# Performance work log

Hardware: AMD Instinct MI355X
Metric: run time of the kernel (lower is better)

The kernel has to match this reference:

```python
import jax, jax.numpy as jnp
import numpy as np

DIM = 1024
NUM_HEADS = 16
HEAD_DIM = DIM // NUM_HEADS
EPS = 1e-6


def _rmsnorm(x, w):
    # x: [B,H,N,D], w: [D]
    var = jnp.mean(x * x, axis=-1, keepdims=True)
    return x * jax.lax.rsqrt(var + EPS) * w


def _rotary(x, cos, sin):
    # x: [B,H,N,D]; cos/sin: [1,1,N,D/2]; complex-pair rotation (llama style)
    x2 = x.reshape(*x.shape[:-1], HEAD_DIM // 2, 2)
    xr, xi = x2[..., 0], x2[..., 1]
    or_ = xr * cos - xi * sin
    oi_ = xr * sin + xi * cos
    return jnp.stack([or_, oi_], axis=-1).reshape(x.shape)


def setup_inputs() -> dict:
    key = jax.random.key(0)
    ks = jax.random.split(key, 6)
    B, N = 2, 2048
    x = jax.random.normal(ks[0], (B, N, DIM), dtype=jnp.float32)
    pos = jax.random.uniform(ks[1], (N, HEAD_DIM // 2), dtype=jnp.float32)  # rotary angles
    s_in = 1.0 / np.sqrt(DIM)
    qkv_w = jax.random.normal(ks[2], (3 * DIM, DIM), dtype=jnp.float32) * s_in
    q_norm_w = jnp.ones((HEAD_DIM,), dtype=jnp.float32)
    k_norm_w = jnp.ones((HEAD_DIM,), dtype=jnp.float32)
    proj_w = jax.random.normal(ks[3], (DIM, DIM), dtype=jnp.float32) * s_in
    proj_b = jnp.zeros((DIM,), dtype=jnp.float32)
    return {"x": x, "pos": pos, "qkv_w": qkv_w, "q_norm_w": q_norm_w,
            "k_norm_w": k_norm_w, "proj_w": proj_w, "proj_b": proj_b}


def reference(x, pos, qkv_w, q_norm_w, k_norm_w, proj_w, proj_b):
    B, N, C = x.shape
    H, D = NUM_HEADS, HEAD_DIM
    scale = D ** -0.5
    # QKV projection: [B,N,3C] -> [3,B,H,N,D]
    qkv = jnp.einsum('bnc,fc->bnf', x, qkv_w)
    qkv = qkv.reshape(B, N, 3, H, D).transpose(2, 0, 3, 1, 4)
    q, k, v = qkv[0], qkv[1], qkv[2]
    # QK RMSNorm over head_dim
    q = _rmsnorm(q, q_norm_w)
    k = _rmsnorm(k, k_norm_w)
    # Rotary embedding (freqs_cis = exp(i * pos))
    cos = jnp.cos(pos)[None, None, :, :]
    sin = jnp.sin(pos)[None, None, :, :]
    q = _rotary(q, cos, sin)
    k = _rotary(k, cos, sin)
    # Scaled dot-product attention (non-causal)
    scores = jnp.einsum('bhnd,bhmd->bhnm', q, k) * scale
    attn = jax.nn.softmax(scores, axis=-1)
    out = jnp.einsum('bhnm,bhmd->bhnd', attn, v)
    out = out.transpose(0, 2, 1, 3).reshape(B, N, C)
    return jnp.einsum('bnc,oc->bno', out, proj_w) + proj_b
```

## Files before the change

### kernel.cpp

```cpp
#include <hip/hip_runtime.h>
#include <hip/hip_bf16.h>

typedef unsigned short ushort_t;
using floatx4 = __attribute__((__ext_vector_type__(4))) float;
using bf16x8  = __attribute__((__ext_vector_type__(8))) __bf16;
using ushort4v = __attribute__((__ext_vector_type__(4))) ushort_t;

__device__ __forceinline__ unsigned int pkbf(float a, float b) {
  __hip_bfloat162 h = __float22bfloat162_rn(make_float2(a, b));
  unsigned int u;
  __builtin_memcpy(&u, &h, 4);
  return u;
}

__device__ __forceinline__ void gl2lds16(const ushort_t* g, ushort_t* l) {
  __builtin_amdgcn_global_load_lds(
      (const __attribute__((address_space(1))) unsigned int*)g,
      (__attribute__((address_space(3))) unsigned int*)l, 16, 0, 0);
}

__global__ void cast_all(const float* __restrict__ x, const float* __restrict__ qw,
                         const float* __restrict__ pw, ushort_t* __restrict__ ob,
                         const float* __restrict__ pos, float* __restrict__ cs) {
  const int T1 = 4096 * 1024, T2 = T1 + 3072 * 1024, T3 = T2 + 1024 * 1024;
  const int tid = blockIdx.x * blockDim.x + threadIdx.x;
  if (tid < 65536) {
    const float a = pos[tid];
    cs[2 * tid]     = __cosf(a);
    cs[2 * tid + 1] = __sinf(a);
  }
  const int i = tid * 4;
  if (i < T3) {
    const float* src = (i < T1) ? (x + i) : (i < T2) ? (qw + (i - T1)) : (pw + (i - T2));
    float4 v = *reinterpret_cast<const float4*>(src);
    uint2 o = make_uint2(pkbf(v.x, v.y), pkbf(v.z, v.w));
    *reinterpret_cast<uint2*>(&ob[i]) = o;
  }
}

__global__ __launch_bounds__(256)
void gemm_qkv_fused(const ushort_t* __restrict__ A, const ushort_t* __restrict__ B,
                    const float* __restrict__ cs,
                    const float* __restrict__ qnw, const float* __restrict__ knw,
                    ushort_t* __restrict__ qr, ushort_t* __restrict__ kr,
                    ushort_t* __restrict__ vt) {
  const int K = 1024;
  __shared__ ushort_t sA[128 * 32];
  __shared__ ushort_t sB[128 * 32];
  __shared__ __align__(16) ushort_t sE[4][4096];
  const int m0 = blockIdx.y * 128, n0 = blockIdx.x * 128;
  const int tid = threadIdx.x;
  const int lane = tid & 63, w = tid >> 6;
  const int wm = (w >> 1) * 64;
  const int grp = lane >> 4, l16 = lane & 15;
  const int r0 = lane >> 2, c0 = (lane & 3) * 8;
  floatx4 acc[4][4] = {};
  for (int k0 = 0; k0 < K; k0 += 32) {
    __syncthreads();
#pragma unroll
    for (int i = 0; i < 2; i++) {
      const int j = w * 2 + i;
      gl2lds16(&A[(size_t)(m0 + j * 16 + r0) * K + k0 + c0], &sA[j * 512]);
      gl2lds16(&B[(size_t)(n0 + j * 16 + r0) * K + k0 + c0], &sB[j * 512]);
    }
    __syncthreads();
    bf16x8 af[4], bfr[4];
#pragma unroll
    for (int i = 0; i < 4; i++)
      af[i] = *reinterpret_cast<const bf16x8*>(&sA[(wm + i * 16 + l16) * 32 + grp * 8]);
#pragma unroll
    for (int i = 0; i < 4; i++)
      bfr[i] = *reinterpret_cast<const bf16x8*>(&sB[((w & 1) * 64 + i * 16 + l16) * 32 + grp * 8]);
#pragma unroll
    for (int i = 0; i < 4; i++)
#pragma unroll
      for (int j = 0; j < 4; j++)
        acc[i][j] = __builtin_amdgcn_mfma_f32_16x16x32_bf16(af[i], bfr[j], acc[i][j], 0, 0, 0);
  }
  const int region = n0 >> 10;
  const int h = ((n0 & 1023) >> 6) + (w & 1);
  const int tbase = m0 + wm;
  const int bb = tbase >> 11;
  const int nwin = tbase & 2047;
  const int q = lane & 7;
  const int lr = lane >> 3;

  if (region < 2) {
    float* sEf = (float*)&sE[w][0];
    const float* nwp = (region == 0) ? qnw : knw;
    const float qmul = (region == 0) ? 0.125f * 1.44269504088896340736f : 1.0f;
    float wgt[8];
    *(float4*)&wgt[0] = *(const float4*)&nwp[q * 8];
    *(float4*)&wgt[4] = *(const float4*)&nwp[q * 8 + 4];
#pragma unroll
    for (int hf = 0; hf < 2; hf++) {
      __syncthreads();
#pragma unroll
      for (int i2 = 0; i2 < 2; i2++)
#pragma unroll
        for (int rr = 0; rr < 4; rr++) {
          const int t2 = i2 * 16 + grp * 4 + rr;
#pragma unroll
          for (int j = 0; j < 4; j++) {
            const int cd = (j * 4 + (l16 >> 2)) ^ (t2 & 15);
            sEf[t2 * 64 + cd * 4 + (l16 & 3)] = acc[hf * 2 + i2][j][rr];
          }
        }
      __syncthreads();
#pragma unroll
      for (int tg = 0; tg < 4; tg++) {
        const int t2 = tg * 8 + lr;
        const int n = (tbase + hf * 32 + t2) & 2047;
        float v0[8];
        const int ck1 = (2 * q) ^ (t2 & 15), ck2 = (2 * q + 1) ^ (t2 & 15);
        *(float4*)&v0[0] = *(const float4*)&sEf[t2 * 64 + ck1 * 4];
        *(float4*)&v0[4] = *(const float4*)&sEf[t2 * 64 + ck2 * 4];
        float ss = 0.f;
#pragma unroll
        for (int e = 0; e < 8; e++) ss += v0[e] * v0[e];
        ss += __shfl_xor(ss, 1); ss += __shfl_xor(ss, 2); ss += __shfl_xor(ss, 4);
        const float rn = rsqrtf(ss * (1.0f / 64.0f) + 1e-6f);
        float4 c01 = *(const float4*)&cs[(n * 32 + q * 4) * 2];
        float4 c23 = *(const float4*)&cs[(n * 32 + q * 4) * 2 + 4];
        float ccv[4] = {c01.x, c01.z, c23.x, c23.z};
        float snv[4] = {c01.y, c01.w, c23.y, c23.w};
        union { unsigned int u32[4]; uint4 v4; } ov;
#pragma unroll
        for (int p = 0; p < 4; p++) {
          const float cc = ccv[p], sn = snv[p];
          const float xr = v0[2 * p] * rn * wgt[2 * p];
          const float xi = v0[2 * p + 1] * rn * wgt[2 * p + 1];
          ov.u32[p] = pkbf((xr * cc - xi * sn) * qmul, (xr * sn + xi * cc) * qmul);
        }
        const size_t rowb = ((size_t)(bb * 16 + h) * 2048 + n) * 64;
        if (region == 0)
          *reinterpret_cast<uint4*>(&qr[rowb + q * 8]) = ov.v4;
        else
          *reinterpret_cast<uint4*>(&kr[rowb + (q ^ (n & 7)) * 8]) = ov.v4;
      }
    }
  } else {
    __syncthreads();
#pragma unroll
    for (int i = 0; i < 4; i++)
#pragma unroll
      for (int j = 0; j < 4; j++) {
        const int d = j * 16 + l16;
        const int ct = (i * 4 + grp) ^ (d & 15);
        uint2 pk = make_uint2(pkbf(acc[i][j][0], acc[i][j][1]),
                              pkbf(acc[i][j][2], acc[i][j][3]));
        *reinterpret_cast<uint2*>(&sE[w][d * 64 + ct * 4]) = pk;
      }
    __syncthreads();
#pragma unroll
    for (int dd = 0; dd < 8; dd++) {
      const int d = dd * 8 + lr;
      const int cta = 8 * (q >> 2) + (q & 3);
      union { ushort4v h[2]; uint4 v4; } ob;
      ob.h[0] = *reinterpret_cast<const ushort4v*>(&sE[w][d * 64 + ((cta ^ (d & 15)) * 4)]);
      ob.h[1] = *reinterpret_cast<const ushort4v*>(&sE[w][d * 64 + (((cta + 4) ^ (d & 15)) * 4)]);
      *reinterpret_cast<uint4*>(
          &vt[((size_t)(bb * 16 + h) * 64 + d) * 2048 + nwin + (q ^ (d & 7)) * 8]) = ob.v4;
    }
  }
}

__global__ __launch_bounds__(256)
void flash_attn(const ushort_t* __restrict__ qr, const ushort_t* __restrict__ kr,
                const ushort_t* __restrict__ vt, ushort_t* __restrict__ aout) {
  const int bh = blockIdx.y;
  const int w = threadIdx.x >> 6, lane = threadIdx.x & 63;
  const int grp = lane >> 4, l16 = lane & 15;
  const int sw = l16 & 7;
  const int q0 = blockIdx.x * 128 + w * 32;
  const size_t hb = (size_t)bh * 2048 * 64;

  __shared__ ushort_t sK[2][128 * 64];
  __shared__ ushort_t sV[2][64 * 128];

  bf16x8 qa[2][2];
#pragma unroll
  for (int f = 0; f < 2; f++) {
    const ushort_t* qp = &qr[hb + (size_t)(q0 + f * 16 + l16) * 64 + grp * 8];
    qa[f][0] = *reinterpret_cast<const bf16x8*>(qp);
    qa[f][1] = *reinterpret_cast<const bf16x8*>(qp + 32);
  }

  floatx4 o[2][4] = {};
  floatx4 ol[2] = {};

  union { ushort_t u[8]; bf16x8 v; } onef;
#pragma unroll
  for (int e = 0; e < 8; e++) onef.u[e] = 0x3F80;

  auto stage = [&](int buf, int k0) {
    const ushort_t* kg = &kr[hb + (size_t)k0 * 64];
#pragma unroll
    for (int i = 0; i < 4; i++) {
      const int j = w * 4 + i;
      gl2lds16(kg + j * 512 + lane * 8, &sK[buf][j * 512]);
    }
#pragma unroll
    for (int i = 0; i < 4; i++) {
      const int d = w * 16 + i * 4;
      gl2lds16(&vt[((size_t)bh * 64 + d + (lane >> 4)) * 2048 + k0 + (lane & 15) * 8],
               &sV[buf][d * 128]);
    }
  };

  stage(0, 0);
  const int g0 = (grp ^ sw) * 8;
  for (int it = 0; it < 16; it++) {
    const int cur = it & 1;
    __syncthreads();
    if (it + 1 < 16) stage(1 - cur, (it + 1) * 128);
#pragma unroll
    for (int hh = 0; hh < 2; hh++) {
      const ushort_t* kb = &sK[cur][hh * 64 * 64];
      const ushort_t* vb = &sV[cur][hh * 64];
      floatx4 s[2][4];
#pragma unroll
      for (int nt = 0; nt < 4; nt++) {
        const ushort_t* kp = kb + (nt * 16 + l16) * 64;
        bf16x8 kf0 = *reinterpret_cast<const bf16x8*>(kp + g0);
        bf16x8 kf1 = *reinterpret_cast<const bf16x8*>(kp + (g0 ^ 32));
#pragma unroll
        for (int f = 0; f < 2; f++) {
          floatx4 acc = {};
          acc = __builtin_amdgcn_mfma_f32_16x16x32_bf16(kf0, qa[f][0], acc, 0, 0, 0);
          acc = __builtin_amdgcn_mfma_f32_16x16x32_bf16(kf1, qa[f][1], acc, 0, 0, 0);
          s[f][nt] = acc;
        }
      }
      union { unsigned int u32[4]; bf16x8 v; } pf[2][2];
#pragma unroll
      for (int f = 0; f < 2; f++) {
        float p[4][4];
#pragma unroll
        for (int nt = 0; nt < 4; nt++)
#pragma unroll
          for (int r = 0; r < 4; r++)
            p[nt][r] = __builtin_amdgcn_exp2f(s[f][nt][r]);
#pragma unroll
        for (int c = 0; c < 2; c++) {
          pf[f][c].u32[0] = pkbf(p[2 * c][0], p[2 * c][1]);
          pf[f][c].u32[1] = pkbf(p[2 * c][2], p[2 * c][3]);
          pf[f][c].u32[2] = pkbf(p[2 * c + 1][0], p[2 * c + 1][1]);
          pf[f][c].u32[3] = pkbf(p[2 * c + 1][2], p[2 * c + 1][3]);
        }
      }
#pragma unroll
      for (int c = 0; c < 2; c++) {
#pragma unroll
        for (int f = 0; f < 2; f++)
          ol[f] = __builtin_amdgcn_mfma_f32_16x16x32_bf16(onef.v, pf[f][c].v, ol[f], 0, 0, 0);
#pragma unroll
        for (int dt = 0; dt < 4; dt++) {
          const bf16x8 vv = *reinterpret_cast<const bf16x8*>(
              vb + (dt * 16 + l16) * 128 + (((c * 4 + grp) ^ sw) << 3));
#pragma unroll
          for (int f = 0; f < 2; f++)
            o[f][dt] = __builtin_amdgcn_mfma_f32_16x16x32_bf16(vv, pf[f][c].v, o[f][dt], 0, 0, 0);
        }
      }
    }
  }
  const int b = bh >> 4, h = bh & 15;
#pragma unroll
  for (int f = 0; f < 2; f++) {
    const float rl = 1.0f / ol[f][0];
    const size_t orow = (size_t)(b * 2048 + q0 + f * 16 + l16) * 1024 + h * 64;
#pragma unroll
    for (int dt = 0; dt < 4; dt++) {
      uint2 ov = make_uint2(pkbf(o[f][dt][0] * rl, o[f][dt][1] * rl),
                            pkbf(o[f][dt][2] * rl, o[f][dt][3] * rl));
      *reinterpret_cast<uint2*>(&aout[orow + dt * 16 + grp * 4]) = ov;
    }
  }
}

__global__ __launch_bounds__(256)
void gemm_proj(const ushort_t* __restrict__ A, const ushort_t* __restrict__ B,
               float* __restrict__ Cout, const float* __restrict__ bias) {
  const int K = 1024, N = 1024;
  __shared__ ushort_t sA[128 * 32];
  __shared__ ushort_t sB[64 * 32];
  __shared__ float sT[4][2048];
  const int m0 = blockIdx.y * 128, n0 = blockIdx.x * 64;
  const int tid = threadIdx.x;
  const int lane = tid & 63, w = tid >> 6;
  const int wm = (w >> 1) * 64, wn = (w & 1) * 32;
  const int grp = lane >> 4, l16 = lane & 15;
  const int r0 = lane >> 2, c0 = (lane & 3) * 8;
  floatx4 acc[4][2] = {};
  for (int k0 = 0; k0 < K; k0 += 32) {
    __syncthreads();
#pragma unroll
    for (int i = 0; i < 2; i++) {
      const int j = w * 2 + i;
      gl2lds16(&A[(size_t)(m0 + j * 16 + r0) * K + k0 + c0], &sA[j * 512]);
    }
    gl2lds16(&B[(size_t)(n0 + w * 16 + r0) * K + k0 + c0], &sB[w * 512]);
    __syncthreads();
    bf16x8 af[4], bfr[2];
#pragma unroll
    for (int i = 0; i < 4; i++)
      af[i] = *reinterpret_cast<const bf16x8*>(&sA[(wm + i * 16 + l16) * 32 + grp * 8]);
#pragma unroll
    for (int j = 0; j < 2; j++)
      bfr[j] = *reinterpret_cast<const bf16x8*>(&sB[(wn + j * 16 + l16) * 32 + grp * 8]);
#pragma unroll
    for (int i = 0; i < 4; i++)
#pragma unroll
      for (int j = 0; j < 2; j++)
        acc[i][j] = __builtin_amdgcn_mfma_f32_16x16x32_bf16(af[i], bfr[j], acc[i][j], 0, 0, 0);
  }
  float bv[2];
#pragma unroll
  for (int j = 0; j < 2; j++) bv[j] = bias[n0 + wn + j * 16 + l16];
#pragma unroll
  for (int i = 0; i < 4; i++)
#pragma unroll
    for (int j = 0; j < 2; j++) {
      const int col = j * 16 + l16, c4 = col >> 2;
#pragma unroll
      for (int rr = 0; rr < 4; rr++) {
        const int row = i * 16 + grp * 4 + rr;
        sT[w][row * 32 + ((c4 ^ (row & 7)) << 2) + (col & 3)] = acc[i][j][rr] + bv[j];
      }
    }
  __builtin_amdgcn_s_waitcnt(0);
  const int lr = lane >> 3, ch = lane & 7;
#pragma unroll
  for (int rg = 0; rg < 8; rg++) {
    const int row = rg * 8 + lr;
    float4 vvv = *(const float4*)&sT[w][row * 32 + ((ch ^ (row & 7)) << 2)];
    *reinterpret_cast<float4*>(&Cout[(size_t)(m0 + wm + row) * N + n0 + wn + ch * 4]) = vvv;
  }
}

extern "C" void kernel_launch(void* const* d_in, const int* in_sizes, int n_in,
                              void* d_out, int out_size, void* d_ws, size_t ws_size,
                              hipStream_t stream) {
  const float* x      = (const float*)d_in[0];
  const float* pos    = (const float*)d_in[1];
  const float* qkv_w  = (const float*)d_in[2];
  const float* q_nw   = (const float*)d_in[3];
  const float* k_nw   = (const float*)d_in[4];
  const float* proj_w = (const float*)d_in[5];
  const float* proj_b = (const float*)d_in[6];
  float* out = (float*)d_out;

  ushort_t* x_b     = (ushort_t*)d_ws;
  ushort_t* qkvw_b  = x_b     + (size_t)4096 * 1024;
  ushort_t* projw_b = qkvw_b  + (size_t)3072 * 1024;
  ushort_t* q_r     = projw_b + (size_t)1024 * 1024;
  ushort_t* k_r     = q_r     + (size_t)32 * 2048 * 64;
  ushort_t* v_t     = k_r     + (size_t)32 * 2048 * 64;
  ushort_t* a_out   = v_t     + (size_t)32 * 2048 * 64;
  float*    cs_tab  = (float*)(a_out + (size_t)4096 * 1024);

  cast_all<<<8388608 / 4 / 256, 256, 0, stream>>>(x, qkv_w, proj_w, x_b, pos, cs_tab);

  gemm_qkv_fused<<<dim3(3072 / 128, 4096 / 128), 256, 0, stream>>>(
      x_b, qkvw_b, cs_tab, q_nw, k_nw, q_r, k_r, v_t);

  flash_attn<<<dim3(2048 / 128, 32), 256, 0, stream>>>(q_r, k_r, v_t, a_out);

  gemm_proj<<<dim3(1024 / 64, 4096 / 128), 256, 0, stream>>>(a_out, projw_b, out, proj_b);
}
```

Baseline: 214.3 us.

## Double GEMM K-step to 64 with XOR-swizzled LDS and alias epilogue scratch

Both the QKV and projection GEMMs now stage 64-wide K slices per iteration instead of 32, which halves the number of barrier pairs in the main loop. The LDS tiles use an XOR swizzle on the 16-byte chunks to avoid bank conflicts on the fragment reads. In the QKV kernel the epilogue scratch now aliases the A/B staging buffers, which cuts the kernel's shared memory footprint. Per-wave epilogue barriers become waitcnt, on the premise that each wave's region is private. The risk is that dropping the block barriers relies on wave-private LDS regions and on LDS ordering within a wave.

```diff
diff --git a/kernel.cpp b/kernel.cpp
--- a/kernel.cpp
+++ b/kernel.cpp
@@ -45,38 +45,50 @@
                     ushort_t* __restrict__ qr, ushort_t* __restrict__ kr,
                     ushort_t* __restrict__ vt) {
   const int K = 1024;
-  __shared__ ushort_t sA[128 * 32];
-  __shared__ ushort_t sB[128 * 32];
-  __shared__ __align__(16) ushort_t sE[4][4096];
+  __shared__ __align__(16) ushort_t smem[16384];
+  ushort_t* sA = smem;
+  ushort_t* sB = smem + 8192;
   const int m0 = blockIdx.y * 128, n0 = blockIdx.x * 128;
   const int tid = threadIdx.x;
   const int lane = tid & 63, w = tid >> 6;
   const int wm = (w >> 1) * 64;
   const int grp = lane >> 4, l16 = lane & 15;
-  const int r0 = lane >> 2, c0 = (lane & 3) * 8;
+  const int r8 = lane >> 3;
+  const int c8 = ((lane & 7) ^ r8) * 8;
   floatx4 acc[4][4] = {};
-  for (int k0 = 0; k0 < K; k0 += 32) {
-    __syncthreads();
-#pragma unroll
-    for (int i = 0; i < 2; i++) {
-      const int j = w * 2 + i;
-      gl2lds16(&A[(size_t)(m0 + j * 16 + r0) * K + k0 + c0], &sA[j * 512]);
-      gl2lds16(&B[(size_t)(n0 + j * 16 + r0) * K + k0 + c0], &sB[j * 512]);
-    }
-    __syncthreads();
-    bf16x8 af[4], bfr[4];
-#pragma unroll
-    for (int i = 0; i < 4; i++)
-      af[i] = *reinterpret_cast<const bf16x8*>(&sA[(wm + i * 16 + l16) * 32 + grp * 8]);
-#pragma unroll
-    for (int i = 0; i < 4; i++)
-      bfr[i] = *reinterpret_cast<const bf16x8*>(&sB[((w & 1) * 64 + i * 16 + l16) * 32 + grp * 8]);
-#pragma unroll
-    for (int i = 0; i < 4; i++)
-#pragma unroll
-      for (int j = 0; j < 4; j++)
-        acc[i][j] = __builtin_amdgcn_mfma_f32_16x16x32_bf16(af[i], bfr[j], acc[i][j], 0, 0, 0);
-  }
+  for (int k0 = 0; k0 < K; k0 += 64) {
+    __syncthreads();
+#pragma unroll
+    for (int i = 0; i < 4; i++) {
+      const int j = w * 4 + i;
+      gl2lds16(&A[(size_t)(m0 + j * 8 + r8) * K + k0 + c8], &sA[j * 512]);
+      gl2lds16(&B[(size_t)(n0 + j * 8 + r8) * K + k0 + c8], &sB[j * 512]);
+    }
+    __syncthreads();
+#pragma unroll
+    for (int kk = 0; kk < 2; kk++) {
+      bf16x8 af[4], bfr[4];
+#pragma unroll
+      for (int i = 0; i < 4; i++) {
+        const int ra = wm + i * 16 + l16;
+        af[i] = *reinterpret_cast<const bf16x8*>(
+            &sA[ra * 64 + (((kk * 4 + grp) ^ (ra & 7)) << 3)]);
+      }
+#pragma unroll
+      for (int i = 0; i < 4; i++) {
+        const int rb = (w & 1) * 64 + i * 16 + l16;
+        bfr[i] = *reinterpret_cast<const bf16x8*>(
+            &sB[rb * 64 + (((kk * 4 + grp) ^ (rb & 7)) << 3)]);
+      }
+#pragma unroll
+      for (int i = 0; i < 4; i++)
+#pragma unroll
+        for (int j = 0; j < 4; j++)
+          acc[i][j] = __builtin_amdgcn_mfma_f32_16x16x32_bf16(af[i], bfr[j], acc[i][j], 0, 0, 0);
+    }
+  }
+  __syncthreads();
+  ushort_t* sE = smem + w * 4096;
   const int region = n0 >> 10;
   const int h = ((n0 & 1023) >> 6) + (w & 1);
   const int tbase = m0 + wm;
@@ -86,7 +98,7 @@
   const int lr = lane >> 3;
 
   if (region < 2) {
-    float* sEf = (float*)&sE[w][0];
+    float* sEf = (float*)sE;
     const float* nwp = (region == 0) ? qnw : knw;
     const float qmul = (region == 0) ? 0.125f * 1.44269504088896340736f : 1.0f;
     float wgt[8];
@@ -94,7 +106,7 @@
     *(float4*)&wgt[4] = *(const float4*)&nwp[q * 8 + 4];
 #pragma unroll
     for (int hf = 0; hf < 2; hf++) {
-      __syncthreads();
+      __builtin_amdgcn_s_waitcnt(0);
 #pragma unroll
       for (int i2 = 0; i2 < 2; i2++)
 #pragma unroll
@@ -106,7 +118,7 @@
             sEf[t2 * 64 + cd * 4 + (l16 & 3)] = acc[hf * 2 + i2][j][rr];
           }
         }
-      __syncthreads();
+      __builtin_amdgcn_s_waitcnt(0);
 #pragma unroll
       for (int tg = 0; tg < 4; tg++) {
         const int t2 = tg * 8 + lr;
@@ -140,7 +152,6 @@
       }
     }
   } else {
-    __syncthreads();
 #pragma unroll
     for (int i = 0; i < 4; i++)
 #pragma unroll
@@ -149,16 +160,16 @@
         const int ct = (i * 4 + grp) ^ (d & 15);
         uint2 pk = make_uint2(pkbf(acc[i][j][0], acc[i][j][1]),
                               pkbf(acc[i][j][2], acc[i][j][3]));
-        *reinterpret_cast<uint2*>(&sE[w][d * 64 + ct * 4]) = pk;
-      }
-    __syncthreads();
+        *reinterpret_cast<uint2*>(&sE[d * 64 + ct * 4]) = pk;
+      }
+    __builtin_amdgcn_s_waitcnt(0);
 #pragma unroll
     for (int dd = 0; dd < 8; dd++) {
       const int d = dd * 8 + lr;
       const int cta = 8 * (q >> 2) + (q & 3);
-      union { ushort4v h[2]; uint4 v4; } ob;
-      ob.h[0] = *reinterpret_cast<const ushort4v*>(&sE[w][d * 64 + ((cta ^ (d & 15)) * 4)]);
-      ob.h[1] = *reinterpret_cast<const ushort4v*>(&sE[w][d * 64 + (((cta + 4) ^ (d & 15)) * 4)]);
+      union { ushort4v hh[2]; uint4 v4; } ob;
+      ob.hh[0] = *reinterpret_cast<const ushort4v*>(&sE[d * 64 + ((cta ^ (d & 15)) * 4)]);
+      ob.hh[1] = *reinterpret_cast<const ushort4v*>(&sE[d * 64 + (((cta + 4) ^ (d & 15)) * 4)]);
       *reinterpret_cast<uint4*>(
           &vt[((size_t)(bb * 16 + h) * 64 + d) * 2048 + nwin + (q ^ (d & 7)) * 8]) = ob.v4;
     }
@@ -283,37 +294,51 @@
 void gemm_proj(const ushort_t* __restrict__ A, const ushort_t* __restrict__ B,
                float* __restrict__ Cout, const float* __restrict__ bias) {
   const int K = 1024, N = 1024;
-  __shared__ ushort_t sA[128 * 32];
-  __shared__ ushort_t sB[64 * 32];
+  __shared__ __align__(16) ushort_t sA[8192];
+  __shared__ __align__(16) ushort_t sB[4096];
   __shared__ float sT[4][2048];
   const int m0 = blockIdx.y * 128, n0 = blockIdx.x * 64;
   const int tid = threadIdx.x;
   const int lane = tid & 63, w = tid >> 6;
   const int wm = (w >> 1) * 64, wn = (w & 1) * 32;
   const int grp = lane >> 4, l16 = lane & 15;
-  const int r0 = lane >> 2, c0 = (lane & 3) * 8;
+  const int r8 = lane >> 3;
+  const int c8 = ((lane & 7) ^ r8) * 8;
   floatx4 acc[4][2] = {};
-  for (int k0 = 0; k0 < K; k0 += 32) {
-    __syncthreads();
+  for (int k0 = 0; k0 < K; k0 += 64) {
+    __syncthreads();
+#pragma unroll
+    for (int i = 0; i < 4; i++) {
+      const int j = w * 4 + i;
+      gl2lds16(&A[(size_t)(m0 + j * 8 + r8) * K + k0 + c8], &sA[j * 512]);
+    }
 #pragma unroll
     for (int i = 0; i < 2; i++) {
       const int j = w * 2 + i;
-      gl2lds16(&A[(size_t)(m0 + j * 16 + r0) * K + k0 + c0], &sA[j * 512]);
-    }
-    gl2lds16(&B[(size_t)(n0 + w * 16 + r0) * K + k0 + c0], &sB[w * 512]);
-    __syncthreads();
-    bf16x8 af[4], bfr[2];
-#pragma unroll
-    for (int i = 0; i < 4; i++)
-      af[i] = *reinterpret_cast<const bf16x8*>(&sA[(wm + i * 16 + l16) * 32 + grp * 8]);
-#pragma unroll
-    for (int j = 0; j < 2; j++)
-      bfr[j] = *reinterpret_cast<const bf16x8*>(&sB[(wn + j * 16 + l16) * 32 + grp * 8]);
-#pragma unroll
-    for (int i = 0; i < 4; i++)
-#pragma unroll
-      for (int j = 0; j < 2; j++)
-        acc[i][j] = __builtin_amdgcn_mfma_f32_16x16x32_bf16(af[i], bfr[j], acc[i][j], 0, 0, 0);
+      gl2lds16(&B[(size_t)(n0 + j * 8 + r8) * K + k0 + c8], &sB[j * 512]);
+    }
+    __syncthreads();
+#pragma unroll
+    for (int kk = 0; kk < 2; kk++) {
+      bf16x8 af[4], bfr[2];
+#pragma unroll
+      for (int i = 0; i < 4; i++) {
+        const int ra = wm + i * 16 + l16;
+        af[i] = *reinterpret_cast<const bf16x8*>(
+            &sA[ra * 64 + (((kk * 4 + grp) ^ (ra & 7)) << 3)]);
+      }
+#pragma unroll
+      for (int j = 0; j < 2; j++) {
+        const int rb = wn + j * 16 + l16;
+        bfr[j] = *reinterpret_cast<const bf16x8*>(
+            &sB[rb * 64 + (((kk * 4 + grp) ^ (rb & 7)) << 3)]);
+      }
+#pragma unroll
+      for (int i = 0; i < 4; i++)
+#pragma unroll
+        for (int j = 0; j < 2; j++)
+          acc[i][j] = __builtin_amdgcn_mfma_f32_16x16x32_bf16(af[i], bfr[j], acc[i][j], 0, 0, 0);
+    }
   }
   float bv[2];
 #pragma unroll
```

Measured after the change: 201.0 us. -6.2%, faster.
